# Kernel tuning notes

Measured on AMD Instinct MI355X. Metric: run time of the kernel, lower is better.

Reference implementation:

```python
import jax, jax.numpy as jnp
import numpy as np

N_HEADS = 16  # matches init_kwargs

def setup_inputs() -> dict:
    key = jax.random.key(0)
    ks = jax.random.split(key, 7)
    B, S, D = 2, 2048, 2048
    return {
        "query": jax.random.normal(ks[0], (B, S, D), jnp.float32),
        "key":   jax.random.normal(ks[1], (B, S, D), jnp.float32),
        "value": jax.random.normal(ks[2], (B, S, D), jnp.float32),
        "Wq": jax.random.normal(ks[3], (D, D), jnp.float32) * 0.02,
        "Wk": jax.random.normal(ks[4], (D, D), jnp.float32) * 0.02,
        "Wv": jax.random.normal(ks[5], (D, D), jnp.float32) * 0.02,
        "Wo": jax.random.normal(ks[6], (D, D), jnp.float32) * 0.02,
        "block_size": 64,
    }

def reference(query, key, value, Wq, Wk, Wv, Wo, block_size):
    # Faithful to the torch module: softmax is applied INDEPENDENTLY per
    # k-block (no online-softmax rescaling) and block outputs are summed.
    B, S, D = query.shape
    H = N_HEADS
    hd = D // H
    nb = S // block_size  # number of k-blocks (S is a multiple of block_size)
    scale = jnp.asarray(np.sqrt(hd), query.dtype)

    # nn.Linear(bias=False): y = x @ W.T
    q = (query @ Wq.T).reshape(B, S, H, hd).transpose(0, 2, 1, 3)  # [B,H,S,hd]
    k = (key   @ Wk.T).reshape(B, S, H, hd).transpose(0, 2, 1, 3)
    v = (value @ Wv.T).reshape(B, S, H, hd).transpose(0, 2, 1, 3)

    kb = k.reshape(B, H, nb, block_size, hd)  # k-blocks
    vb = v.reshape(B, H, nb, block_size, hd)

    scores = jnp.einsum('bhsd,bhnkd->bhsnk', q, kb) / scale  # [B,H,S,nb,bs]
    attn = jax.nn.softmax(scores, axis=-1)  # per-block softmax (as in source)
    out = jnp.einsum('bhsnk,bhnkd->bhsd', attn, vb)  # sum over blocks

    attn_weights = attn.reshape(B, H, S, S)  # full materialized attn matrix
    out = out.transpose(0, 2, 1, 3).reshape(B, S, D) @ Wo.T
    return out, attn_weights
```

## Files before the change

kernel.cpp:

```cpp
#include <hip/hip_runtime.h>

typedef unsigned short u16;
typedef unsigned int u32;
typedef __attribute__((ext_vector_type(8))) __bf16 bf16x8;
typedef __attribute__((ext_vector_type(4))) float f32x4;

__device__ __forceinline__ void gl_lds16(const void* g, void* l) {
  __builtin_amdgcn_global_load_lds((__attribute__((address_space(1))) void*)g,
                                   (__attribute__((address_space(3))) void*)l,
                                   16, 0, 0);
}

__device__ __forceinline__ u16 f2bf(float f) {
  u32 x = __builtin_bit_cast(u32, f);
  return (u16)((x + 0x7fffu + ((x >> 16) & 1u)) >> 16);
}

__global__ __launch_bounds__(256) void cvt_all(
    const float* __restrict__ q, const float* __restrict__ k, const float* __restrict__ v,
    const float* __restrict__ wq, const float* __restrict__ wk, const float* __restrict__ wv,
    const float* __restrict__ wo,
    u16* __restrict__ xq, u16* __restrict__ xk, u16* __restrict__ xv,
    u16* __restrict__ owq, u16* __restrict__ owk, u16* __restrict__ owv,
    u16* __restrict__ owo) {
  int bid = blockIdx.x;
  const float* src;
  u16* dst;
  int chunk;
  if (bid < 12288) {
    int t = bid >> 12;
    chunk = bid & 4095;
    src = (t == 0) ? q : (t == 1) ? k : v;
    dst = (t == 0) ? xq : (t == 1) ? xk : xv;
  } else {
    int b2 = bid - 12288;
    int t = b2 >> 11;
    chunk = b2 & 2047;
    src = (t == 0) ? wq : (t == 1) ? wk : (t == 2) ? wv : wo;
    dst = (t == 0) ? owq : (t == 1) ? owk : (t == 2) ? owv : owo;
  }
  int i = (chunk * 256 + (int)threadIdx.x) * 8;
  const float4* p = (const float4*)(src + i);
  float4 a = p[0], b = p[1];
  uint4 u;
  u.x = f2bf(a.x) | ((u32)f2bf(a.y) << 16);
  u.y = f2bf(a.z) | ((u32)f2bf(a.w) << 16);
  u.z = f2bf(b.x) | ((u32)f2bf(b.y) << 16);
  u.w = f2bf(b.z) | ((u32)f2bf(b.w) << 16);
  *(uint4*)(dst + i) = u;
}

template <bool F32OUT>
__device__ __forceinline__ void gemm_body(const u16* __restrict__ A, const u16* __restrict__ B,
                                          void* __restrict__ Cptr, int m0, int n0, int N, int K,
                                          u16* As, u16* Bs) {
  const int tid = threadIdx.x;
  const int lane = tid & 63, w = tid >> 6;
  const int wm = (w & 1) * 64, wn = (w >> 1) * 64;
  const int fm = lane & 15, quad = lane >> 4;
  const int sr = lane >> 2, sc = lane & 3;
  f32x4 acc[4][4] = {};
  for (int k0 = 0; k0 < K; k0 += 32) {
    __syncthreads();
    for (int i = w; i < 8; i += 4) {
      int r = i * 16 + sr;
      int ca = sc ^ ((r >> 1) & 3);
      gl_lds16(A + (size_t)(m0 + r) * K + k0 + ca * 8, &As[i * 512]);
      gl_lds16(B + (size_t)(n0 + r) * K + k0 + ca * 8, &Bs[i * 512]);
    }
    __syncthreads();
    bf16x8 af[4], bfr[4];
#pragma unroll
    for (int t = 0; t < 4; t++) {
      int ra = wm + t * 16 + fm;
      af[t] = *(const bf16x8*)&As[ra * 32 + ((quad ^ ((ra >> 1) & 3)) << 3)];
      int rb = wn + t * 16 + fm;
      bfr[t] = *(const bf16x8*)&Bs[rb * 32 + ((quad ^ ((rb >> 1) & 3)) << 3)];
    }
#pragma unroll
    for (int mt = 0; mt < 4; mt++)
#pragma unroll
      for (int nt = 0; nt < 4; nt++)
        acc[mt][nt] = __builtin_amdgcn_mfma_f32_16x16x32_bf16(af[mt], bfr[nt], acc[mt][nt], 0, 0, 0);
  }
  const int er = quad * 4;
#pragma unroll
  for (int mt = 0; mt < 4; mt++)
#pragma unroll
    for (int nt = 0; nt < 4; nt++)
#pragma unroll
      for (int r = 0; r < 4; r++) {
        size_t idx = (size_t)(m0 + wm + mt * 16 + er + r) * N + (n0 + wn + nt * 16 + fm);
        if (F32OUT) ((float*)Cptr)[idx] = acc[mt][nt][r];
        else        ((u16*)Cptr)[idx] = f2bf(acc[mt][nt][r]);
      }
}

__global__ __launch_bounds__(256, 2)
void gemm_qkv(const u16* __restrict__ Xq, const u16* __restrict__ Wqb, u16* __restrict__ Qb,
              const u16* __restrict__ Xk, const u16* __restrict__ Wkb, u16* __restrict__ Kb,
              const u16* __restrict__ Xv, const u16* __restrict__ Wvb, u16* __restrict__ Vt) {
  __shared__ u16 As[128 * 32];
  __shared__ u16 Bs[128 * 32];
  const int bid = blockIdx.x, z = blockIdx.y;
  const u16 *A, *B;
  u16* C;
  int N, m0, n0;
  if (z == 0) {
    A = Xq; B = Wqb; C = Qb; N = 2048;
    m0 = (bid >> 4) << 7; n0 = (bid & 15) << 7;
  } else if (z == 1) {
    A = Xk; B = Wkb; C = Kb; N = 2048;
    m0 = (bid >> 4) << 7; n0 = (bid & 15) << 7;
  } else {
    A = Wvb; B = Xv; C = Vt; N = 4096;
    m0 = (bid >> 5) << 7; n0 = (bid & 31) << 7;
  }
  gemm_body<false>(A, B, C, m0, n0, N, 2048, As, Bs);
}

__global__ __launch_bounds__(256, 2)
void gemm_out(const u16* __restrict__ A, const u16* __restrict__ B, float* __restrict__ C) {
  __shared__ u16 As[128 * 32];
  __shared__ u16 Bs[128 * 32];
  gemm_body<true>(A, B, C, (int)(blockIdx.y << 7), (int)(blockIdx.x << 7), 2048, 2048, As, Bs);
}

__global__ __launch_bounds__(256, 2)
void attn_kernel(const u16* __restrict__ Q, const u16* __restrict__ Kmat,
                 const u16* __restrict__ Vt, float* __restrict__ attn_out,
                 u16* __restrict__ ctx) {
  __shared__ u16 Ks[2][64 * 128];
  __shared__ u16 Vts[2][128 * 64];
  __shared__ u16 Ps[128 * 64];
  const int tid = threadIdx.x, lane = tid & 63, w = tid >> 6;
  const int qt = blockIdx.x, h = blockIdx.y, b = blockIdx.z;
  const int q0 = qt * 128;
  const int fm = lane & 15, quad = lane >> 4;
  const float c_e2 = 0.088388347648318447f * 1.4426950408889634f;

  bf16x8 qf[2][4];
  {
    const u16* Qg = Q + (size_t)(b * 2048 + q0 + w * 32 + fm) * 2048 + h * 128;
#pragma unroll
    for (int mt = 0; mt < 2; mt++)
#pragma unroll
      for (int kt = 0; kt < 4; kt++)
        qf[mt][kt] = *(const bf16x8*)(Qg + (size_t)mt * 16 * 2048 + kt * 32 + quad * 8);
  }
  f32x4 cacc[2][8] = {};
  const u16* Kg = Kmat + (size_t)b * 2048 * 2048 + h * 128;
  const u16* Vg = Vt + (size_t)(h * 128) * 4096 + b * 2048;
  const int krl = lane >> 4, kcl = lane & 15;
  const int vrl = lane >> 3, vcl = lane & 7;

#define STAGE(buf, kbb)                                                              \
  for (int i = w; i < 16; i += 4) {                                                  \
    int rk = i * 4 + krl;                                                            \
    int ck = kcl ^ (rk & 15);                                                        \
    gl_lds16(Kg + (size_t)((kbb) * 64 + rk) * 2048 + ck * 8, &Ks[(buf)][i * 512]);   \
    int rv = i * 8 + vrl;                                                            \
    int cv = vcl ^ (rv & 7);                                                         \
    gl_lds16(Vg + (size_t)rv * 4096 + (kbb) * 64 + cv * 8, &Vts[(buf)][i * 512]);    \
  }

  STAGE(0, 0)
  asm volatile("s_waitcnt vmcnt(0)" ::: "memory");
  __builtin_amdgcn_s_barrier();

  for (int kb = 0; kb < 32; kb++) {
    const int cur = kb & 1;
    if (kb < 31) { STAGE(cur ^ 1, kb + 1) }

    f32x4 sacc[2][4] = {};
#pragma unroll
    for (int kt = 0; kt < 4; kt++) {
      bf16x8 kf[4];
#pragma unroll
      for (int nt = 0; nt < 4; nt++) {
        int rk = nt * 16 + fm;
        int ck = (kt * 4 + quad) ^ (rk & 15);
        kf[nt] = *(const bf16x8*)&Ks[cur][rk * 128 + ck * 8];
      }
      __builtin_amdgcn_s_setprio(1);
#pragma unroll
      for (int mt = 0; mt < 2; mt++)
#pragma unroll
        for (int nt = 0; nt < 4; nt++)
          sacc[mt][nt] = __builtin_amdgcn_mfma_f32_16x16x32_bf16(qf[mt][kt], kf[nt], sacc[mt][nt], 0, 0, 0);
      __builtin_amdgcn_s_setprio(0);
    }

#pragma unroll
    for (int mt = 0; mt < 2; mt++)
#pragma unroll
      for (int r = 0; r < 4; r++) {
        float v0 = sacc[mt][0][r], v1 = sacc[mt][1][r], v2 = sacc[mt][2][r], v3 = sacc[mt][3][r];
        float mx = fmaxf(fmaxf(v0, v1), fmaxf(v2, v3));
        mx = fmaxf(mx, __shfl_xor(mx, 1));
        mx = fmaxf(mx, __shfl_xor(mx, 2));
        mx = fmaxf(mx, __shfl_xor(mx, 4));
        mx = fmaxf(mx, __shfl_xor(mx, 8));
        float e0 = exp2f((v0 - mx) * c_e2);
        float e1 = exp2f((v1 - mx) * c_e2);
        float e2 = exp2f((v2 - mx) * c_e2);
        float e3 = exp2f((v3 - mx) * c_e2);
        float s = e0 + e1 + e2 + e3;
        s += __shfl_xor(s, 1);
        s += __shfl_xor(s, 2);
        s += __shfl_xor(s, 4);
        s += __shfl_xor(s, 8);
        float inv = __builtin_amdgcn_rcpf(s);
        float p0 = e0 * inv, p1 = e1 * inv, p2 = e2 * inv, p3 = e3 * inv;
        int row = w * 32 + mt * 16 + quad * 4 + r;
        size_t ob = ((size_t)((b * 16 + h) * 2048 + q0 + row)) * 2048 + kb * 64;
        attn_out[ob + fm] = p0;
        attn_out[ob + 16 + fm] = p1;
        attn_out[ob + 32 + fm] = p2;
        attn_out[ob + 48 + fm] = p3;
        int rw7 = row & 7, fh = fm >> 3, fl = fm & 7;
        u16* pp = &Ps[row * 64];
        pp[(((0 + fh) ^ rw7) << 3) + fl] = f2bf(p0);
        pp[(((2 + fh) ^ rw7) << 3) + fl] = f2bf(p1);
        pp[(((4 + fh) ^ rw7) << 3) + fl] = f2bf(p2);
        pp[(((6 + fh) ^ rw7) << 3) + fl] = f2bf(p3);
      }

#pragma unroll
    for (int kt = 0; kt < 2; kt++) {
      bf16x8 pa[2], vb[8];
#pragma unroll
      for (int mt = 0; mt < 2; mt++) {
        int rp = w * 32 + mt * 16 + fm;
        int cp = (kt * 4 + quad) ^ (rp & 7);
        pa[mt] = *(const bf16x8*)&Ps[rp * 64 + cp * 8];
      }
#pragma unroll
      for (int nt = 0; nt < 8; nt++) {
        int rv = nt * 16 + fm;
        int cv = (kt * 4 + quad) ^ (rv & 7);
        vb[nt] = *(const bf16x8*)&Vts[cur][rv * 64 + cv * 8];
      }
      __builtin_amdgcn_s_setprio(1);
#pragma unroll
      for (int mt = 0; mt < 2; mt++)
#pragma unroll
        for (int nt = 0; nt < 8; nt++)
          cacc[mt][nt] = __builtin_amdgcn_mfma_f32_16x16x32_bf16(pa[mt], vb[nt], cacc[mt][nt], 0, 0, 0);
      __builtin_amdgcn_s_setprio(0);
    }

    if (kb < 31) {
      asm volatile("s_waitcnt vmcnt(0)" ::: "memory");
      __builtin_amdgcn_s_barrier();
    }
  }
#undef STAGE

#pragma unroll
  for (int mt = 0; mt < 2; mt++)
#pragma unroll
    for (int nt = 0; nt < 8; nt++)
#pragma unroll
      for (int r = 0; r < 4; r++) {
        int row = q0 + w * 32 + mt * 16 + quad * 4 + r;
        int col = h * 128 + nt * 16 + fm;
        ctx[(size_t)(b * 2048 + row) * 2048 + col] = f2bf(cacc[mt][nt][r]);
      }
}

extern "C" void kernel_launch(void* const* d_in, const int* in_sizes, int n_in,
                              void* d_out, int out_size, void* d_ws, size_t ws_size,
                              hipStream_t stream) {
  const float* query = (const float*)d_in[0];
  const float* key   = (const float*)d_in[1];
  const float* value = (const float*)d_in[2];
  const float* Wq = (const float*)d_in[3];
  const float* Wk = (const float*)d_in[4];
  const float* Wv = (const float*)d_in[5];
  const float* Wo = (const float*)d_in[6];

  float* out  = (float*)d_out;
  float* attn = out + (size_t)8388608;

  u16* ws  = (u16*)d_ws;
  u16* wqb = ws;
  u16* wkb = wqb + 4194304;
  u16* wvb = wkb + 4194304;
  u16* wob = wvb + 4194304;
  u16* Qb  = wob + 4194304;
  u16* Kb  = Qb + 8388608;
  u16* Vtb = Kb + 8388608;
  u16* ctx = Vtb + 8388608;
  u16* Xq = (u16*)attn;
  u16* Xk = Xq + 8388608;
  u16* Xv = Xk + 8388608;

  cvt_all<<<20480, 256, 0, stream>>>(query, key, value, Wq, Wk, Wv, Wo,
                                     Xq, Xk, Xv, wqb, wkb, wvb, wob);

  gemm_qkv<<<dim3(512, 3, 1), 256, 0, stream>>>(Xq, wqb, Qb, Xk, wkb, Kb, Xv, wvb, Vtb);

  attn_kernel<<<dim3(16, 16, 2), 256, 0, stream>>>(Qb, Kb, Vtb, attn, ctx);

  gemm_out<<<dim3(16, 32, 1), 256, 0, stream>>>(ctx, wob, out);
}
```

Before: 996.5 us.

## Split attention across eight waves and remap block IDs for XCD locality

The attention kernel now runs 512 threads per block, with each wave owning 16 query rows instead of 32. This halves per-wave registers and work and adds more waves to hide the latency of the attention-matrix stores. All three kernels also remap the flat block index so that consecutive work tiles land on the same XCD, which should improve L2 reuse of shared K/V and weight tiles. In exchange, every wave still reads the full K and V tiles from LDS, so LDS read traffic per output doubles, and the launch bound of 4 blocks per CU may limit registers.

After: 980.8 us. Within noise of the previous version (-1.6%).

```diff
diff --git a/kernel.cpp b/kernel.cpp
--- a/kernel.cpp
+++ b/kernel.cpp
@@ -102,7 +102,9 @@
               const u16* __restrict__ Xv, const u16* __restrict__ Wvb, u16* __restrict__ Vt) {
   __shared__ u16 As[128 * 32];
   __shared__ u16 Bs[128 * 32];
-  const int bid = blockIdx.x, z = blockIdx.y;
+  const int flat = blockIdx.x + (blockIdx.y << 9);
+  const int work = (flat & 7) * 192 + (flat >> 3);
+  const int z = work >> 9, bid = work & 511;
   const u16 *A, *B;
   u16* C;
   int N, m0, n0;
@@ -123,10 +125,13 @@
 void gemm_out(const u16* __restrict__ A, const u16* __restrict__ B, float* __restrict__ C) {
   __shared__ u16 As[128 * 32];
   __shared__ u16 Bs[128 * 32];
-  gemm_body<true>(A, B, C, (int)(blockIdx.y << 7), (int)(blockIdx.x << 7), 2048, 2048, As, Bs);
-}
-
-__global__ __launch_bounds__(256, 2)
+  const int flat = blockIdx.x + (blockIdx.y << 4);
+  const int work = ((flat & 7) << 6) + (flat >> 3);
+  const int m0 = (work >> 4) << 7, n0 = (work & 15) << 7;
+  gemm_body<true>(A, B, C, m0, n0, 2048, 2048, As, Bs);
+}
+
+__global__ __launch_bounds__(512, 4)
 void attn_kernel(const u16* __restrict__ Q, const u16* __restrict__ Kmat,
                  const u16* __restrict__ Vt, float* __restrict__ attn_out,
                  u16* __restrict__ ctx) {
@@ -134,28 +139,28 @@
   __shared__ u16 Vts[2][128 * 64];
   __shared__ u16 Ps[128 * 64];
   const int tid = threadIdx.x, lane = tid & 63, w = tid >> 6;
-  const int qt = blockIdx.x, h = blockIdx.y, b = blockIdx.z;
+  const int flat = blockIdx.x + (blockIdx.y << 4) + (blockIdx.z << 8);
+  const int work = ((flat & 7) << 6) + (flat >> 3);
+  const int qt = work & 15, h = (work >> 4) & 15, b = work >> 8;
   const int q0 = qt * 128;
   const int fm = lane & 15, quad = lane >> 4;
   const float c_e2 = 0.088388347648318447f * 1.4426950408889634f;
 
-  bf16x8 qf[2][4];
+  bf16x8 qf[4];
   {
-    const u16* Qg = Q + (size_t)(b * 2048 + q0 + w * 32 + fm) * 2048 + h * 128;
-#pragma unroll
-    for (int mt = 0; mt < 2; mt++)
-#pragma unroll
-      for (int kt = 0; kt < 4; kt++)
-        qf[mt][kt] = *(const bf16x8*)(Qg + (size_t)mt * 16 * 2048 + kt * 32 + quad * 8);
-  }
-  f32x4 cacc[2][8] = {};
+    const u16* Qg = Q + (size_t)(b * 2048 + q0 + w * 16 + fm) * 2048 + h * 128;
+#pragma unroll
+    for (int kt = 0; kt < 4; kt++)
+      qf[kt] = *(const bf16x8*)(Qg + kt * 32 + quad * 8);
+  }
+  f32x4 cacc[8] = {};
   const u16* Kg = Kmat + (size_t)b * 2048 * 2048 + h * 128;
   const u16* Vg = Vt + (size_t)(h * 128) * 4096 + b * 2048;
   const int krl = lane >> 4, kcl = lane & 15;
   const int vrl = lane >> 3, vcl = lane & 7;
 
 #define STAGE(buf, kbb)                                                              \
-  for (int i = w; i < 16; i += 4) {                                                  \
+  for (int i = w; i < 16; i += 8) {                                                  \
     int rk = i * 4 + krl;                                                            \
     int ck = kcl ^ (rk & 15);                                                        \
     gl_lds16(Kg + (size_t)((kbb) * 64 + rk) * 2048 + ck * 8, &Ks[(buf)][i * 512]);   \
@@ -172,7 +177,7 @@
     const int cur = kb & 1;
     if (kb < 31) { STAGE(cur ^ 1, kb + 1) }
 
-    f32x4 sacc[2][4] = {};
+    f32x4 sacc[4] = {};
 #pragma unroll
     for (int kt = 0; kt < 4; kt++) {
       bf16x8 kf[4];
@@ -184,56 +189,51 @@
       }
       __builtin_amdgcn_s_setprio(1);
 #pragma unroll
-      for (int mt = 0; mt < 2; mt++)
-#pragma unroll
-        for (int nt = 0; nt < 4; nt++)
-          sacc[mt][nt] = __builtin_amdgcn_mfma_f32_16x16x32_bf16(qf[mt][kt], kf[nt], sacc[mt][nt], 0, 0, 0);
+      for (int nt = 0; nt < 4; nt++)
+        sacc[nt] = __builtin_amdgcn_mfma_f32_16x16x32_bf16(qf[kt], kf[nt], sacc[nt], 0, 0, 0);
       __builtin_amdgcn_s_setprio(0);
     }
 
 #pragma unroll
-    for (int mt = 0; mt < 2; mt++)
-#pragma unroll
-      for (int r = 0; r < 4; r++) {
-        float v0 = sacc[mt][0][r], v1 = sacc[mt][1][r], v2 = sacc[mt][2][r], v3 = sacc[mt][3][r];
-        float mx = fmaxf(fmaxf(v0, v1), fmaxf(v2, v3));
-        mx = fmaxf(mx, __shfl_xor(mx, 1));
-        mx = fmaxf(mx, __shfl_xor(mx, 2));
-        mx = fmaxf(mx, __shfl_xor(mx, 4));
-        mx = fmaxf(mx, __shfl_xor(mx, 8));
-        float e0 = exp2f((v0 - mx) * c_e2);
-        float e1 = exp2f((v1 - mx) * c_e2);
-        float e2 = exp2f((v2 - mx) * c_e2);
-        float e3 = exp2f((v3 - mx) * c_e2);
-        float s = e0 + e1 + e2 + e3;
-        s += __shfl_xor(s, 1);
-        s += __shfl_xor(s, 2);
-        s += __shfl_xor(s, 4);
-        s += __shfl_xor(s, 8);
-        float inv = __builtin_amdgcn_rcpf(s);
-        float p0 = e0 * inv, p1 = e1 * inv, p2 = e2 * inv, p3 = e3 * inv;
-        int row = w * 32 + mt * 16 + quad * 4 + r;
-        size_t ob = ((size_t)((b * 16 + h) * 2048 + q0 + row)) * 2048 + kb * 64;
-        attn_out[ob + fm] = p0;
-        attn_out[ob + 16 + fm] = p1;
-        attn_out[ob + 32 + fm] = p2;
-        attn_out[ob + 48 + fm] = p3;
-        int rw7 = row & 7, fh = fm >> 3, fl = fm & 7;
-        u16* pp = &Ps[row * 64];
-        pp[(((0 + fh) ^ rw7) << 3) + fl] = f2bf(p0);
-        pp[(((2 + fh) ^ rw7) << 3) + fl] = f2bf(p1);
-        pp[(((4 + fh) ^ rw7) << 3) + fl] = f2bf(p2);
-        pp[(((6 + fh) ^ rw7) << 3) + fl] = f2bf(p3);
-      }
+    for (int r = 0; r < 4; r++) {
+      float v0 = sacc[0][r], v1 = sacc[1][r], v2 = sacc[2][r], v3 = sacc[3][r];
+      float mx = fmaxf(fmaxf(v0, v1), fmaxf(v2, v3));
+      mx = fmaxf(mx, __shfl_xor(mx, 1));
+      mx = fmaxf(mx, __shfl_xor(mx, 2));
+      mx = fmaxf(mx, __shfl_xor(mx, 4));
+      mx = fmaxf(mx, __shfl_xor(mx, 8));
+      float e0 = exp2f((v0 - mx) * c_e2);
+      float e1 = exp2f((v1 - mx) * c_e2);
+      float e2 = exp2f((v2 - mx) * c_e2);
+      float e3 = exp2f((v3 - mx) * c_e2);
+      float s = e0 + e1 + e2 + e3;
+      s += __shfl_xor(s, 1);
+      s += __shfl_xor(s, 2);
+      s += __shfl_xor(s, 4);
+      s += __shfl_xor(s, 8);
+      float inv = __builtin_amdgcn_rcpf(s);
+      float p0 = e0 * inv, p1 = e1 * inv, p2 = e2 * inv, p3 = e3 * inv;
+      int row = w * 16 + quad * 4 + r;
+      size_t ob = ((size_t)((b * 16 + h) * 2048 + q0 + row)) * 2048 + kb * 64;
+      attn_out[ob + fm] = p0;
+      attn_out[ob + 16 + fm] = p1;
+      attn_out[ob + 32 + fm] = p2;
+      attn_out[ob + 48 + fm] = p3;
+      int rw7 = row & 7, fh = fm >> 3, fl = fm & 7;
+      u16* pp = &Ps[row * 64];
+      pp[(((0 + fh) ^ rw7) << 3) + fl] = f2bf(p0);
+      pp[(((2 + fh) ^ rw7) << 3) + fl] = f2bf(p1);
+      pp[(((4 + fh) ^ rw7) << 3) + fl] = f2bf(p2);
+      pp[(((6 + fh) ^ rw7) << 3) + fl] = f2bf(p3);
+    }
 
 #pragma unroll
     for (int kt = 0; kt < 2; kt++) {
-      bf16x8 pa[2], vb[8];
-#pragma unroll
-      for (int mt = 0; mt < 2; mt++) {
-        int rp = w * 32 + mt * 16 + fm;
+      bf16x8 pa, vb[8];
+      {
+        int rp = w * 16 + fm;
         int cp = (kt * 4 + quad) ^ (rp & 7);
-        pa[mt] = *(const bf16x8*)&Ps[rp * 64 + cp * 8];
+        pa = *(const bf16x8*)&Ps[rp * 64 + cp * 8];
       }
 #pragma unroll
       for (int nt = 0; nt < 8; nt++) {
@@ -243,10 +243,8 @@
       }
       __builtin_amdgcn_s_setprio(1);
 #pragma unroll
-      for (int mt = 0; mt < 2; mt++)
-#pragma unroll
-        for (int nt = 0; nt < 8; nt++)
-          cacc[mt][nt] = __builtin_amdgcn_mfma_f32_16x16x32_bf16(pa[mt], vb[nt], cacc[mt][nt], 0, 0, 0);
+      for (int nt = 0; nt < 8; nt++)
+        cacc[nt] = __builtin_amdgcn_mfma_f32_16x16x32_bf16(pa, vb[nt], cacc[nt], 0, 0, 0);
       __builtin_amdgcn_s_setprio(0);
     }
 
@@ -258,15 +256,13 @@
 #undef STAGE
 
 #pragma unroll
-  for (int mt = 0; mt < 2; mt++)
-#pragma unroll
-    for (int nt = 0; nt < 8; nt++)
-#pragma unroll
-      for (int r = 0; r < 4; r++) {
-        int row = q0 + w * 32 + mt * 16 + quad * 4 + r;
-        int col = h * 128 + nt * 16 + fm;
-        ctx[(size_t)(b * 2048 + row) * 2048 + col] = f2bf(cacc[mt][nt][r]);
-      }
+  for (int nt = 0; nt < 8; nt++)
+#pragma unroll
+    for (int r = 0; r < 4; r++) {
+      int row = q0 + w * 16 + quad * 4 + r;
+      int col = h * 128 + nt * 16 + fm;
+      ctx[(size_t)(b * 2048 + row) * 2048 + col] = f2bf(cacc[nt][r]);
+    }
 }
 
 extern "C" void kernel_launch(void* const* d_in, const int* in_sizes, int n_in,
@@ -301,7 +297,7 @@
 
   gemm_qkv<<<dim3(512, 3, 1), 256, 0, stream>>>(Xq, wqb, Qb, Xk, wkb, Kb, Xv, wvb, Vtb);
 
-  attn_kernel<<<dim3(16, 16, 2), 256, 0, stream>>>(Qb, Kb, Vtb, attn, ctx);
+  attn_kernel<<<dim3(16, 16, 2), 512, 0, stream>>>(Qb, Kb, Vtb, attn, ctx);
 
   gemm_out<<<dim3(16, 32, 1), 256, 0, stream>>>(ctx, wob, out);
 }
```
